# Optimization experiments

Measured on AMD Instinct MI355X. Metric: run time of the kernel, lower is better.

## Reference

```python
import jax, jax.numpy as jnp
import numpy as np
import math


def setup_inputs() -> dict:
    key = jax.random.key(0)
    ks = jax.random.split(key, 5)
    B, C, E = 4, 2048, 1024
    max_len = 2048
    s = 1.0 / math.sqrt(E)
    return {
        "x": jax.random.normal(ks[0], (B, C, E), dtype=jnp.float32),
        "W_q": jax.random.normal(ks[1], (E, E), dtype=jnp.float32) * s,
        "W_k": jax.random.normal(ks[2], (E, E), dtype=jnp.float32) * s,
        "W_v": jax.random.normal(ks[3], (E, E), dtype=jnp.float32) * s,
        "rel_bias": jax.random.normal(ks[4], (2 * max_len - 1, 1), dtype=jnp.float32),
        "max_len": max_len,
    }


def reference(x, W_q, W_k, W_v, rel_bias, max_len):
    B, C, E = x.shape
    # nn.Linear(bias=False): y = x @ W.T
    Q = jnp.einsum("bce,fe->bcf", x, W_q)
    K = jnp.einsum("bce,fe->bcf", x, W_k)
    V = jnp.einsum("bce,fe->bcf", x, W_v)
    scores = jnp.einsum("bqe,bke->bqk", Q, K) / math.sqrt(E)
    pos = jnp.arange(C)
    rel_dist = jnp.clip(pos[None, :] - pos[:, None] + (max_len - 1), 0, 2 * max_len - 2)
    bias = rel_bias[rel_dist, 0]  # [C, C]
    scores = scores + bias[None, :, :]
    weights = jax.nn.softmax(scores, axis=-1)
    out = jnp.einsum("bqk,bke->bqe", weights, V)
    return out, weights
```

## Files before the change

kernel.cpp:

```cpp
#include <hip/hip_runtime.h>
#include <hip/hip_bf16.h>
#include <math.h>

typedef __attribute__((ext_vector_type(8))) short short8;
typedef __attribute__((ext_vector_type(4))) short short4v;
typedef __attribute__((ext_vector_type(4))) float f32x4;

static __device__ __forceinline__ short f2bf(float f) {
  union { float f; unsigned u; } x;
  x.f = f;
  unsigned r = x.u + 0x7fffu + ((x.u >> 16) & 1u);
  return (short)(r >> 16);
}

#define GLD16(g, l)                                                   \
  __builtin_amdgcn_global_load_lds(                                   \
      (const __attribute__((address_space(1))) void*)(g),             \
      (__attribute__((address_space(3))) void*)(l), 16, 0, 0)
#define BAR() asm volatile("s_barrier" ::: "memory")
#define VMCNT4() asm volatile("s_waitcnt vmcnt(4)" ::: "memory")
#define VMCNT0() asm volatile("s_waitcnt vmcnt(0)" ::: "memory")

__global__ __launch_bounds__(256) void cvt_all(
    const float* __restrict__ x, const float* __restrict__ wq,
    const float* __restrict__ wk, const float* __restrict__ wv,
    short* __restrict__ xb, short* __restrict__ wqb,
    short* __restrict__ wkb, short* __restrict__ wvb, int n0, int n1) {
  int i = blockIdx.x * 256 + threadIdx.x;
  const float* src; short* dst; int off;
  if (i < n0) { src = x; dst = xb; off = i; }
  else if (i < n0 + n1) { src = wq; dst = wqb; off = i - n0; }
  else if (i < n0 + 2 * n1) { src = wk; dst = wkb; off = i - n0 - n1; }
  else if (i < n0 + 3 * n1) { src = wv; dst = wvb; off = i - n0 - 2 * n1; }
  else return;
  const float4* p = (const float4*)src + (size_t)off * 2;
  float4 a = p[0], b = p[1];
  short8 o;
  o[0] = f2bf(a.x); o[1] = f2bf(a.y); o[2] = f2bf(a.z); o[3] = f2bf(a.w);
  o[4] = f2bf(b.x); o[5] = f2bf(b.y); o[6] = f2bf(b.z); o[7] = f2bf(b.w);
  *((short8*)dst + off) = o;
}

template <int MODE>
__global__ __launch_bounds__(256, 3) void gemm_oc(
    const short* __restrict__ A, const short* __restrict__ Bt,
    void* __restrict__ C0, void* __restrict__ C1, void* __restrict__ C2,
    const float* __restrict__ rel_bias,
    int N, int K, long aZ, long bZ, long cZ, int Cdim, float scale, int ml) {
  __shared__ short sA[3][128 * 32];
  __shared__ short sB[3][128 * 32];
  const int tid = threadIdx.x, lane = tid & 63, wid = tid >> 6;

  const int gx = gridDim.x, gy = gridDim.y;
  const int nwg = gx * gy * (int)gridDim.z;
  const int f = ((int)blockIdx.z * gy + (int)blockIdx.y) * gx + (int)blockIdx.x;
  const int qq = nwg >> 3, rr = nwg & 7;
  const int xcd = f & 7, pos = f >> 3;
  const int lg = (xcd < rr ? xcd * (qq + 1) : rr * (qq + 1) + (xcd - rr) * qq) + pos;
  const int z = lg / (gx * gy);
  const int rem = lg - z * (gx * gy);
  const int bx = rem / gy, by = rem - bx * gy;

  const short* Az = A + (size_t)z * aZ;
  const short* Bz = Bt + (size_t)z * bZ;
  const int brow = bx * 128, bcol = by * 128;
  const int wr = wid >> 1, wc = wid & 1;
  const int lrow = lane & 15, kg = lane >> 4;

  const int t4 = tid >> 2;
  const int logslot = (tid & 3) ^ ((tid >> 3) & 3);
  const short* aSrc0 = Az + (size_t)(brow + t4) * K + logslot * 8;
  const short* aSrc1 = Az + (size_t)(brow + 64 + t4) * K + logslot * 8;
  const short* bSrc0 = Bz + (size_t)(bcol + t4) * K + logslot * 8;
  const short* bSrc1 = Bz + (size_t)(bcol + 64 + t4) * K + logslot * 8;
  const int d0 = wid * 512, d1 = 2048 + wid * 512;

  const int kOff = (kg ^ ((lrow >> 1) & 3)) * 8;
  const int aBase = (wr * 64 + lrow) * 32 + kOff;
  const int bBase = (wc * 64 + lrow) * 32 + kOff;

  short8 a[4], b[4];
  f32x4 acc[4][4] = {};

  short *pa0 = &sA[0][0], *pa1 = &sA[1][0], *pa2 = &sA[2][0];
  short *pb0 = &sB[0][0], *pb1 = &sB[1][0], *pb2 = &sB[2][0];

#define STG(PA, PB, T)                                    \
  do {                                                    \
    GLD16(aSrc0 + (size_t)(T) * 32, (PA) + d0);           \
    GLD16(aSrc1 + (size_t)(T) * 32, (PA) + d1);           \
    GLD16(bSrc0 + (size_t)(T) * 32, (PB) + d0);           \
    GLD16(bSrc1 + (size_t)(T) * 32, (PB) + d1);           \
  } while (0)
#define RD(PA, PB)                                                  \
  do {                                                              \
    _Pragma("unroll") for (int m = 0; m < 4; ++m)                   \
        a[m] = *(const short8*)&(PA)[aBase + m * 512];              \
    _Pragma("unroll") for (int n = 0; n < 4; ++n)                   \
        b[n] = *(const short8*)&(PB)[bBase + n * 512];              \
  } while (0)
#define MFMA16()                                                              \
  do {                                                                        \
    __builtin_amdgcn_s_setprio(1);                                            \
    _Pragma("unroll") for (int m = 0; m < 4; ++m)                             \
        _Pragma("unroll") for (int n = 0; n < 4; ++n)                         \
            acc[m][n] = __builtin_amdgcn_mfma_f32_16x16x32_bf16(              \
                a[m], b[n], acc[m][n], 0, 0, 0);                              \
    __builtin_amdgcn_s_setprio(0);                                            \
  } while (0)
#define ROT()                                                    \
  do {                                                           \
    short* q;                                                    \
    q = pa0; pa0 = pa1; pa1 = pa2; pa2 = q;                      \
    q = pb0; pb0 = pb1; pb1 = pb2; pb2 = q;                      \
  } while (0)

  STG(pa0, pb0, 0);
  STG(pa1, pb1, 1);

  const int NT = K >> 5;
  for (int t = 0; t < NT - 2; ++t) {
    VMCNT4();
    BAR();
    RD(pa0, pb0);
    STG(pa2, pb2, t + 2);
    MFMA16();
    ROT();
  }
  VMCNT4();
  BAR();
  RD(pa0, pb0);
  MFMA16();
  ROT();
  VMCNT0();
  BAR();
  RD(pa0, pb0);
  MFMA16();

#pragma unroll
  for (int m = 0; m < 4; ++m) {
#pragma unroll
    for (int n = 0; n < 4; ++n) {
#pragma unroll
      for (int r = 0; r < 4; ++r) {
        float v = acc[m][n][r];
        int gr = brow + wr * 64 + m * 16 + kg * 4 + r;
        int gc = bcol + wc * 64 + n * 16 + lrow;
        if constexpr (MODE == 2) {
          int idx = gc - gr + (ml - 1);
          idx = min(max(idx, 0), 2 * ml - 2);
          ((float*)C0 + (size_t)z * cZ)[(size_t)gr * N + gc] =
              v * scale + rel_bias[idx];
        } else if constexpr (MODE == 3) {
          ((float*)C0 + (size_t)z * cZ)[(size_t)gr * N + gc] = v;
        } else {
          int s = gc >> 10, cc = gc & 1023;
          short* dst = (s == 0) ? (short*)C0 : (s == 1) ? (short*)C1 : (short*)C2;
          dst[(size_t)gr * 1024 + cc] = f2bf(v);
        }
      }
    }
  }
#undef STG
#undef RD
#undef MFMA16
#undef ROT
}

__global__ __launch_bounds__(256) void transpose_v(const short* __restrict__ vin,
                                                   short* __restrict__ vout,
                                                   int Cd, int E) {
  __shared__ short t[64][72];
  const int c0 = blockIdx.x * 64, e0 = blockIdx.y * 64, b = blockIdx.z;
  const int tid = threadIdx.x;
  const int cr = tid >> 2;
  const int ec = (tid & 3) * 16;
  const short* src = vin + ((size_t)b * Cd + c0 + cr) * E + e0 + ec;
  short8 v0 = *(const short8*)src;
  short8 v1 = *(const short8*)(src + 8);
#pragma unroll
  for (int j = 0; j < 8; ++j) t[ec + j][cr] = v0[j];
#pragma unroll
  for (int j = 0; j < 8; ++j) t[ec + 8 + j][cr] = v1[j];
  __syncthreads();
  const int er = tid >> 2;
  const int cc = (tid & 3) * 16;
  short* dst = vout + ((size_t)b * E + e0 + er) * Cd + c0 + cc;
  *(short8*)dst = *(const short8*)&t[er][cc];
  *(short8*)(dst + 8) = *(const short8*)&t[er][cc + 8];
}

__global__ __launch_bounds__(256) void softmax_rows(float* __restrict__ w,
                                                    short* __restrict__ wb, int Cd) {
  const size_t row = blockIdx.x;
  float4* p = (float4*)(w + row * (size_t)Cd);
  const int tid = threadIdx.x;
  float4 v0 = p[tid];
  float4 v1 = p[tid + 256];
  float mx = fmaxf(fmaxf(fmaxf(v0.x, v0.y), fmaxf(v0.z, v0.w)),
                   fmaxf(fmaxf(v1.x, v1.y), fmaxf(v1.z, v1.w)));
#pragma unroll
  for (int o = 32; o; o >>= 1) mx = fmaxf(mx, __shfl_xor(mx, o));
  __shared__ float red[8];
  const int wv = tid >> 6;
  if ((tid & 63) == 0) red[wv] = mx;
  __syncthreads();
  mx = fmaxf(fmaxf(red[0], red[1]), fmaxf(red[2], red[3]));
  v0.x = __expf(v0.x - mx); v0.y = __expf(v0.y - mx);
  v0.z = __expf(v0.z - mx); v0.w = __expf(v0.w - mx);
  v1.x = __expf(v1.x - mx); v1.y = __expf(v1.y - mx);
  v1.z = __expf(v1.z - mx); v1.w = __expf(v1.w - mx);
  float s = v0.x + v0.y + v0.z + v0.w + v1.x + v1.y + v1.z + v1.w;
#pragma unroll
  for (int o = 32; o; o >>= 1) s += __shfl_xor(s, o);
  if ((tid & 63) == 0) red[4 + wv] = s;
  __syncthreads();
  s = red[4] + red[5] + red[6] + red[7];
  float inv = 1.0f / s;
  v0.x *= inv; v0.y *= inv; v0.z *= inv; v0.w *= inv;
  v1.x *= inv; v1.y *= inv; v1.z *= inv; v1.w *= inv;
  p[tid] = v0;
  p[tid + 256] = v1;
  short4v b0, b1;
  b0[0] = f2bf(v0.x); b0[1] = f2bf(v0.y); b0[2] = f2bf(v0.z); b0[3] = f2bf(v0.w);
  b1[0] = f2bf(v1.x); b1[1] = f2bf(v1.y); b1[2] = f2bf(v1.z); b1[3] = f2bf(v1.w);
  short* wrow = wb + row * (size_t)Cd;
  *(short4v*)&wrow[tid * 4] = b0;
  *(short4v*)&wrow[1024 + tid * 4] = b1;
}

extern "C" void kernel_launch(void* const* d_in, const int* in_sizes, int n_in,
                              void* d_out, int out_size, void* d_ws, size_t ws_size,
                              hipStream_t stream) {
  const float* x = (const float*)d_in[0];
  const float* Wq = (const float*)d_in[1];
  const float* Wk = (const float*)d_in[2];
  const float* Wv = (const float*)d_in[3];
  const float* rb = (const float*)d_in[4];

  const int E = 1024;
  const int Mt = in_sizes[0] / E;
  const int Cd = out_size / Mt - E;
  const int B = Mt / Cd;
  const int ml = (in_sizes[4] + 1) / 2;
  const float scale = 1.0f / sqrtf((float)E);

  short* xb = (short*)d_ws;
  short* wqb = xb + (size_t)Mt * E;
  short* wkb = wqb + (size_t)E * E;
  short* wvb = wkb + (size_t)E * E;
  short* Qb = wvb + (size_t)E * E;
  short* Kb = Qb + (size_t)Mt * E;
  short* Vrow = Kb + (size_t)Mt * E;
  short* Vt = xb;
  short* wbf = Qb;

  float* outp = (float*)d_out;
  float* wts = outp + (size_t)Mt * E;

  const int n0 = (Mt * E) / 8, n1 = (E * E) / 8;
  cvt_all<<<(n0 + 3 * n1 + 255) / 256, 256, 0, stream>>>(
      x, Wq, Wk, Wv, xb, wqb, wkb, wvb, n0, n1);

  dim3 blk(256);
  gemm_oc<4><<<dim3(Mt / 128, 3 * E / 128, 1), blk, 0, stream>>>(
      xb, wqb, Qb, Kb, Vrow, nullptr, 3 * E, E, 0, 0, 0, Cd, 0.f, ml);
  gemm_oc<2><<<dim3(Cd / 128, Cd / 128, B), blk, 0, stream>>>(
      Qb, Kb, wts, nullptr, nullptr, rb, Cd, E, (long)Cd * E, (long)Cd * E,
      (long)Cd * Cd, Cd, scale, ml);
  softmax_rows<<<Mt, 256, 0, stream>>>(wts, wbf, Cd);
  transpose_v<<<dim3(Cd / 64, E / 64, B), 256, 0, stream>>>(Vrow, Vt, Cd, E);
  gemm_oc<3><<<dim3(Cd / 128, E / 128, B), blk, 0, stream>>>(
      wbf, Vt, outp, nullptr, nullptr, nullptr, E, Cd, (long)Cd * Cd,
      (long)E * Cd, (long)Cd * E, Cd, 0.f, ml);
}
```

Before: 198.3 us.

## Load GEMM B operand directly from global into registers, bypassing LDS

The GEMM kernel now stages only the A tile through LDS with a triple buffer. Each wave loads its B fragments straight from global memory into double-buffered registers one k-step ahead, and the main loop is unrolled by two with adjusted vmcnt waits. This halves LDS traffic and LDS footprint and removes the B-side LDS reads. In exchange, B rows shared across waves are fetched redundantly from global memory or L2, global loads are 16-byte strided, and register pressure rises.

```diff
diff --git a/kernel.cpp b/kernel.cpp
--- a/kernel.cpp
+++ b/kernel.cpp
@@ -18,8 +18,9 @@
       (const __attribute__((address_space(1))) void*)(g),             \
       (__attribute__((address_space(3))) void*)(l), 16, 0, 0)
 #define BAR() asm volatile("s_barrier" ::: "memory")
-#define VMCNT4() asm volatile("s_waitcnt vmcnt(4)" ::: "memory")
-#define VMCNT0() asm volatile("s_waitcnt vmcnt(0)" ::: "memory")
+#define VM6() asm volatile("s_waitcnt vmcnt(6)" ::: "memory")
+#define VM4() asm volatile("s_waitcnt vmcnt(4)" ::: "memory")
+#define FENCE() asm volatile("" ::: "memory")
 
 __global__ __launch_bounds__(256) void cvt_all(
     const float* __restrict__ x, const float* __restrict__ wq,
@@ -42,13 +43,12 @@
 }
 
 template <int MODE>
-__global__ __launch_bounds__(256, 3) void gemm_oc(
+__global__ __launch_bounds__(256, 3) void gemm_bd(
     const short* __restrict__ A, const short* __restrict__ Bt,
     void* __restrict__ C0, void* __restrict__ C1, void* __restrict__ C2,
     const float* __restrict__ rel_bias,
     int N, int K, long aZ, long bZ, long cZ, int Cdim, float scale, int ml) {
   __shared__ short sA[3][128 * 32];
-  __shared__ short sB[3][128 * 32];
   const int tid = threadIdx.x, lane = tid & 63, wid = tid >> 6;
 
   const int gx = gridDim.x, gy = gridDim.y;
@@ -71,71 +71,84 @@
   const int logslot = (tid & 3) ^ ((tid >> 3) & 3);
   const short* aSrc0 = Az + (size_t)(brow + t4) * K + logslot * 8;
   const short* aSrc1 = Az + (size_t)(brow + 64 + t4) * K + logslot * 8;
-  const short* bSrc0 = Bz + (size_t)(bcol + t4) * K + logslot * 8;
-  const short* bSrc1 = Bz + (size_t)(bcol + 64 + t4) * K + logslot * 8;
   const int d0 = wid * 512, d1 = 2048 + wid * 512;
 
   const int kOff = (kg ^ ((lrow >> 1) & 3)) * 8;
   const int aBase = (wr * 64 + lrow) * 32 + kOff;
-  const int bBase = (wc * 64 + lrow) * 32 + kOff;
-
-  short8 a[4], b[4];
+
+  const short* bP[4];
+#pragma unroll
+  for (int n = 0; n < 4; ++n)
+    bP[n] = Bz + (size_t)(bcol + wc * 64 + n * 16 + lrow) * K + kg * 8;
+
+  short8 a[4], b0[4], b1[4];
   f32x4 acc[4][4] = {};
 
   short *pa0 = &sA[0][0], *pa1 = &sA[1][0], *pa2 = &sA[2][0];
-  short *pb0 = &sB[0][0], *pb1 = &sB[1][0], *pb2 = &sB[2][0];
-
-#define STG(PA, PB, T)                                    \
+
+#define STG_A(PA, T)                                      \
   do {                                                    \
     GLD16(aSrc0 + (size_t)(T) * 32, (PA) + d0);           \
     GLD16(aSrc1 + (size_t)(T) * 32, (PA) + d1);           \
-    GLD16(bSrc0 + (size_t)(T) * 32, (PB) + d0);           \
-    GLD16(bSrc1 + (size_t)(T) * 32, (PB) + d1);           \
-  } while (0)
-#define RD(PA, PB)                                                  \
+  } while (0)
+#define RD_A(PA)                                                    \
   do {                                                              \
     _Pragma("unroll") for (int m = 0; m < 4; ++m)                   \
         a[m] = *(const short8*)&(PA)[aBase + m * 512];              \
+  } while (0)
+#define LDB(BB, T)                                                  \
+  do {                                                              \
     _Pragma("unroll") for (int n = 0; n < 4; ++n)                   \
-        b[n] = *(const short8*)&(PB)[bBase + n * 512];              \
-  } while (0)
-#define MFMA16()                                                              \
+        BB[n] = *(const short8*)(bP[n] + (size_t)(T) * 32);         \
+  } while (0)
+#define MFMA16(BB)                                                            \
   do {                                                                        \
     __builtin_amdgcn_s_setprio(1);                                            \
     _Pragma("unroll") for (int m = 0; m < 4; ++m)                             \
         _Pragma("unroll") for (int n = 0; n < 4; ++n)                         \
             acc[m][n] = __builtin_amdgcn_mfma_f32_16x16x32_bf16(              \
-                a[m], b[n], acc[m][n], 0, 0, 0);                              \
+                a[m], BB[n], acc[m][n], 0, 0, 0);                             \
     __builtin_amdgcn_s_setprio(0);                                            \
   } while (0)
-#define ROT()                                                    \
+#define ROT3()                                                   \
   do {                                                           \
-    short* q;                                                    \
-    q = pa0; pa0 = pa1; pa1 = pa2; pa2 = q;                      \
-    q = pb0; pb0 = pb1; pb1 = pb2; pb2 = q;                      \
-  } while (0)
-
-  STG(pa0, pb0, 0);
-  STG(pa1, pb1, 1);
+    short* q = pa0; pa0 = pa1; pa1 = pa2; pa2 = q;               \
+  } while (0)
+
+  STG_A(pa0, 0); STG_A(pa1, 1);
+  FENCE();
+  LDB(b0, 0);
 
   const int NT = K >> 5;
-  for (int t = 0; t < NT - 2; ++t) {
-    VMCNT4();
+  for (int t = 0; t < NT - 2; t += 2) {
+    VM6();
     BAR();
-    RD(pa0, pb0);
-    STG(pa2, pb2, t + 2);
-    MFMA16();
-    ROT();
+    RD_A(pa0);
+    STG_A(pa2, t + 2);
+    FENCE();
+    LDB(b1, t + 1);
+    MFMA16(b0);
+    ROT3();
+    VM6();
+    BAR();
+    RD_A(pa0);
+    STG_A(pa2, t + 3);
+    FENCE();
+    LDB(b0, t + 2);
+    MFMA16(b1);
+    ROT3();
   }
-  VMCNT4();
+  VM6();
   BAR();
-  RD(pa0, pb0);
-  MFMA16();
-  ROT();
-  VMCNT0();
+  RD_A(pa0);
+  FENCE();
+  LDB(b1, NT - 1);
+  MFMA16(b0);
+  ROT3();
+  VM4();
   BAR();
-  RD(pa0, pb0);
-  MFMA16();
+  RD_A(pa0);
+  MFMA16(b1);
 
 #pragma unroll
   for (int m = 0; m < 4; ++m) {
@@ -161,10 +174,11 @@
       }
     }
   }
-#undef STG
-#undef RD
+#undef STG_A
+#undef RD_A
+#undef LDB
 #undef MFMA16
-#undef ROT
+#undef ROT3
 }
 
 __global__ __launch_bounds__(256) void transpose_v(const short* __restrict__ vin,
@@ -263,14 +277,14 @@
       x, Wq, Wk, Wv, xb, wqb, wkb, wvb, n0, n1);
 
   dim3 blk(256);
-  gemm_oc<4><<<dim3(Mt / 128, 3 * E / 128, 1), blk, 0, stream>>>(
+  gemm_bd<4><<<dim3(Mt / 128, 3 * E / 128, 1), blk, 0, stream>>>(
       xb, wqb, Qb, Kb, Vrow, nullptr, 3 * E, E, 0, 0, 0, Cd, 0.f, ml);
-  gemm_oc<2><<<dim3(Cd / 128, Cd / 128, B), blk, 0, stream>>>(
+  gemm_bd<2><<<dim3(Cd / 128, Cd / 128, B), blk, 0, stream>>>(
       Qb, Kb, wts, nullptr, nullptr, rb, Cd, E, (long)Cd * E, (long)Cd * E,
       (long)Cd * Cd, Cd, scale, ml);
   softmax_rows<<<Mt, 256, 0, stream>>>(wts, wbf, Cd);
   transpose_v<<<dim3(Cd / 64, E / 64, B), 256, 0, stream>>>(Vrow, Vt, Cd, E);
-  gemm_oc<3><<<dim3(Cd / 128, E / 128, B), blk, 0, stream>>>(
+  gemm_bd<3><<<dim3(Cd / 128, E / 128, B), blk, 0, stream>>>(
       wbf, Vt, outp, nullptr, nullptr, nullptr, E, Cd, (long)Cd * Cd,
       (long)E * Cd, (long)Cd * E, Cd, 0.f, ml);
 }
```

Result: slower. 308.1 us (+55.4%).

## Enlarge GEMM tile to 256x128 with each wave owning full column span

Applied to the files above, without the earlier changes.

Changes the GEMM block tile from 128x128 to 256x128. Each of four waves now computes a 64x128 sub-tile (4x8 MFMA fragments) instead of 64x64, and the staging loads, LDS buffers, vmcnt waits and launch grids are adjusted to match. The aim is better operand reuse per LDS read and fewer global loads per FLOP. In exchange it doubles accumulator registers, lowers the occupancy target to 2 blocks, increases LDS use, and halves the number of workgroups, which can leave CUs idle on smaller grids.

```diff
diff --git a/kernel.cpp b/kernel.cpp
--- a/kernel.cpp
+++ b/kernel.cpp
@@ -18,7 +18,7 @@
       (const __attribute__((address_space(1))) void*)(g),             \
       (__attribute__((address_space(3))) void*)(l), 16, 0, 0)
 #define BAR() asm volatile("s_barrier" ::: "memory")
-#define VMCNT4() asm volatile("s_waitcnt vmcnt(4)" ::: "memory")
+#define VMCNT6() asm volatile("s_waitcnt vmcnt(6)" ::: "memory")
 #define VMCNT0() asm volatile("s_waitcnt vmcnt(0)" ::: "memory")
 
 __global__ __launch_bounds__(256) void cvt_all(
@@ -42,12 +42,12 @@
 }
 
 template <int MODE>
-__global__ __launch_bounds__(256, 3) void gemm_oc(
+__global__ __launch_bounds__(256, 2) void gemm_wt(
     const short* __restrict__ A, const short* __restrict__ Bt,
     void* __restrict__ C0, void* __restrict__ C1, void* __restrict__ C2,
     const float* __restrict__ rel_bias,
     int N, int K, long aZ, long bZ, long cZ, int Cdim, float scale, int ml) {
-  __shared__ short sA[3][128 * 32];
+  __shared__ short sA[3][256 * 32];
   __shared__ short sB[3][128 * 32];
   const int tid = threadIdx.x, lane = tid & 63, wid = tid >> 6;
 
@@ -63,47 +63,52 @@
 
   const short* Az = A + (size_t)z * aZ;
   const short* Bz = Bt + (size_t)z * bZ;
-  const int brow = bx * 128, bcol = by * 128;
-  const int wr = wid >> 1, wc = wid & 1;
+  const int brow = bx * 256, bcol = by * 128;
   const int lrow = lane & 15, kg = lane >> 4;
 
   const int t4 = tid >> 2;
   const int logslot = (tid & 3) ^ ((tid >> 3) & 3);
-  const short* aSrc0 = Az + (size_t)(brow + t4) * K + logslot * 8;
-  const short* aSrc1 = Az + (size_t)(brow + 64 + t4) * K + logslot * 8;
-  const short* bSrc0 = Bz + (size_t)(bcol + t4) * K + logslot * 8;
-  const short* bSrc1 = Bz + (size_t)(bcol + 64 + t4) * K + logslot * 8;
-  const int d0 = wid * 512, d1 = 2048 + wid * 512;
+  const short* aSrc[4];
+#pragma unroll
+  for (int c = 0; c < 4; ++c)
+    aSrc[c] = Az + (size_t)(brow + c * 64 + t4) * K + logslot * 8;
+  const short* bSrc[2];
+#pragma unroll
+  for (int c = 0; c < 2; ++c)
+    bSrc[c] = Bz + (size_t)(bcol + c * 64 + t4) * K + logslot * 8;
+  const int dW = wid * 512;
 
   const int kOff = (kg ^ ((lrow >> 1) & 3)) * 8;
-  const int aBase = (wr * 64 + lrow) * 32 + kOff;
-  const int bBase = (wc * 64 + lrow) * 32 + kOff;
-
-  short8 a[4], b[4];
-  f32x4 acc[4][4] = {};
+  const int aBase = (wid * 64 + lrow) * 32 + kOff;
+  const int bBase = lrow * 32 + kOff;
+
+  short8 a[4], b[8];
+  f32x4 acc[4][8] = {};
 
   short *pa0 = &sA[0][0], *pa1 = &sA[1][0], *pa2 = &sA[2][0];
   short *pb0 = &sB[0][0], *pb1 = &sB[1][0], *pb2 = &sB[2][0];
 
-#define STG(PA, PB, T)                                    \
-  do {                                                    \
-    GLD16(aSrc0 + (size_t)(T) * 32, (PA) + d0);           \
-    GLD16(aSrc1 + (size_t)(T) * 32, (PA) + d1);           \
-    GLD16(bSrc0 + (size_t)(T) * 32, (PB) + d0);           \
-    GLD16(bSrc1 + (size_t)(T) * 32, (PB) + d1);           \
+#define STG(PA, PB, T)                                               \
+  do {                                                               \
+    GLD16(aSrc[0] + (size_t)(T) * 32, (PA) + 0 * 2048 + dW);         \
+    GLD16(aSrc[1] + (size_t)(T) * 32, (PA) + 1 * 2048 + dW);         \
+    GLD16(aSrc[2] + (size_t)(T) * 32, (PA) + 2 * 2048 + dW);         \
+    GLD16(aSrc[3] + (size_t)(T) * 32, (PA) + 3 * 2048 + dW);         \
+    GLD16(bSrc[0] + (size_t)(T) * 32, (PB) + 0 * 2048 + dW);         \
+    GLD16(bSrc[1] + (size_t)(T) * 32, (PB) + 1 * 2048 + dW);         \
   } while (0)
 #define RD(PA, PB)                                                  \
   do {                                                              \
     _Pragma("unroll") for (int m = 0; m < 4; ++m)                   \
         a[m] = *(const short8*)&(PA)[aBase + m * 512];              \
-    _Pragma("unroll") for (int n = 0; n < 4; ++n)                   \
+    _Pragma("unroll") for (int n = 0; n < 8; ++n)                   \
         b[n] = *(const short8*)&(PB)[bBase + n * 512];              \
   } while (0)
-#define MFMA16()                                                              \
+#define MFMA32()                                                              \
   do {                                                                        \
     __builtin_amdgcn_s_setprio(1);                                            \
     _Pragma("unroll") for (int m = 0; m < 4; ++m)                             \
-        _Pragma("unroll") for (int n = 0; n < 4; ++n)                         \
+        _Pragma("unroll") for (int n = 0; n < 8; ++n)                         \
             acc[m][n] = __builtin_amdgcn_mfma_f32_16x16x32_bf16(              \
                 a[m], b[n], acc[m][n], 0, 0, 0);                              \
     __builtin_amdgcn_s_setprio(0);                                            \
@@ -120,32 +125,32 @@
 
   const int NT = K >> 5;
   for (int t = 0; t < NT - 2; ++t) {
-    VMCNT4();
+    VMCNT6();
     BAR();
     RD(pa0, pb0);
     STG(pa2, pb2, t + 2);
-    MFMA16();
+    MFMA32();
     ROT();
   }
-  VMCNT4();
+  VMCNT6();
   BAR();
   RD(pa0, pb0);
-  MFMA16();
+  MFMA32();
   ROT();
   VMCNT0();
   BAR();
   RD(pa0, pb0);
-  MFMA16();
+  MFMA32();
 
 #pragma unroll
   for (int m = 0; m < 4; ++m) {
 #pragma unroll
-    for (int n = 0; n < 4; ++n) {
+    for (int n = 0; n < 8; ++n) {
 #pragma unroll
       for (int r = 0; r < 4; ++r) {
         float v = acc[m][n][r];
-        int gr = brow + wr * 64 + m * 16 + kg * 4 + r;
-        int gc = bcol + wc * 64 + n * 16 + lrow;
+        int gr = brow + wid * 64 + m * 16 + kg * 4 + r;
+        int gc = bcol + n * 16 + lrow;
         if constexpr (MODE == 2) {
           int idx = gc - gr + (ml - 1);
           idx = min(max(idx, 0), 2 * ml - 2);
@@ -163,7 +168,7 @@
   }
 #undef STG
 #undef RD
-#undef MFMA16
+#undef MFMA32
 #undef ROT
 }
 
@@ -263,14 +268,14 @@
       x, Wq, Wk, Wv, xb, wqb, wkb, wvb, n0, n1);
 
   dim3 blk(256);
-  gemm_oc<4><<<dim3(Mt / 128, 3 * E / 128, 1), blk, 0, stream>>>(
+  gemm_wt<4><<<dim3(Mt / 256, 3 * E / 128, 1), blk, 0, stream>>>(
       xb, wqb, Qb, Kb, Vrow, nullptr, 3 * E, E, 0, 0, 0, Cd, 0.f, ml);
-  gemm_oc<2><<<dim3(Cd / 128, Cd / 128, B), blk, 0, stream>>>(
+  gemm_wt<2><<<dim3(Cd / 256, Cd / 128, B), blk, 0, stream>>>(
       Qb, Kb, wts, nullptr, nullptr, rb, Cd, E, (long)Cd * E, (long)Cd * E,
       (long)Cd * Cd, Cd, scale, ml);
   softmax_rows<<<Mt, 256, 0, stream>>>(wts, wbf, Cd);
   transpose_v<<<dim3(Cd / 64, E / 64, B), 256, 0, stream>>>(Vrow, Vt, Cd, E);
-  gemm_oc<3><<<dim3(Cd / 128, E / 128, B), blk, 0, stream>>>(
+  gemm_wt<3><<<dim3(Cd / 256, E / 128, B), blk, 0, stream>>>(
       wbf, Vt, outp, nullptr, nullptr, nullptr, E, Cd, (long)Cd * Cd,
       (long)E * Cd, (long)Cd * E, Cd, 0.f, ml);
 }
```

Result: faster. 193.8 us, median of 3 (-2.3%).
